# Kernel tuning notes

Measured on AMD Instinct MI355X. Metric: run time of the kernel, lower is better.

## Reference

```python
import jax, jax.numpy as jnp
import numpy as np

def setup_inputs() -> dict:
    key = jax.random.key(0)
    k1, k2 = jax.random.split(key)
    user_embeddings = jax.random.normal(k1, (1024, 64), dtype=jnp.float32)
    movie_embeddings = jax.random.normal(k2, (50000, 64), dtype=jnp.float32)
    return {"user_embeddings": user_embeddings, "movie_embeddings": movie_embeddings}

def reference(user_embeddings, movie_embeddings):
    # square_of_sum[b,m] = (sum_k u[b,k] m[m,k])^2
    square_of_sum = jnp.matmul(user_embeddings, movie_embeddings.T) ** 2
    # sum_of_square[b,m] = sum_k (u[b,k] m[m,k])^2 = (u^2) @ (m^2)^T
    # Algebraically identical to the original's broadcast (B, M, D) intermediate,
    # but computed as a second GEMM on squared embeddings.
    sum_of_square = jnp.matmul(user_embeddings ** 2, (movie_embeddings ** 2).T)
    interaction = 0.5 * (square_of_sum - sum_of_square)
    return interaction
```

## Files before the change

kernel.cpp:

```cpp
#include <hip/hip_runtime.h>

typedef short short8 __attribute__((ext_vector_type(8)));
typedef float f32x4 __attribute__((ext_vector_type(4)));

#define DK 64
#define BM 64
#define BN 128

__device__ __forceinline__ short f2bf(float x) {
    unsigned u = __builtin_bit_cast(unsigned, x);
    unsigned r = (u + 0x7fffu + ((u >> 16) & 1u)) >> 16;
    return (short)r;
}

__device__ __forceinline__ short8 sq8(short8 v) {
    short8 r;
#pragma unroll
    for (int i = 0; i < 8; ++i) {
        unsigned u = ((unsigned)(unsigned short)v[i]) << 16;
        float f = __builtin_bit_cast(float, u);
        unsigned p = __builtin_bit_cast(unsigned, f * f);
        r[i] = (short)((p + 0x8000u) >> 16);
    }
    return r;
}

__device__ __forceinline__ void gl_lds16(const void* g, void* l) {
    __builtin_amdgcn_global_load_lds(
        (const __attribute__((address_space(1))) unsigned int*)g,
        (__attribute__((address_space(3))) unsigned int*)l, 16, 0, 0);
}

__global__ __launch_bounds__(256)
void fm_convert(const float* __restrict__ U, const float* __restrict__ M,
                short* __restrict__ ws, int NU, int NM, int NUP, int NMP) {
    int id = blockIdx.x * blockDim.x + threadIdx.x;
    int total = (NUP + NMP) * 8;
    if (id >= total) return;
    int rowg = id >> 3;
    int p = id & 7;
    const float* src; short* dv; int row, nvalid;
    if (rowg < NUP) {
        row = rowg; src = U; dv = ws; nvalid = NU;
    } else {
        row = rowg - NUP; src = M;
        dv = ws + (size_t)NUP * DK; nvalid = NM;
    }
    short8 v8 = {0,0,0,0,0,0,0,0};
    if (row < nvalid) {
        const int cp = p ^ (row & 7);
        const float* s = src + (size_t)row * DK + cp * 8;
        float4 a = *(const float4*)(s);
        float4 b = *(const float4*)(s + 4);
        v8 = (short8){ f2bf(a.x), f2bf(a.y), f2bf(a.z), f2bf(a.w),
                       f2bf(b.x), f2bf(b.y), f2bf(b.z), f2bf(b.w) };
    }
    *(short8*)(dv + (size_t)row * DK + p * 8) = v8;
}

__global__ __launch_bounds__(256, 6)
void fm_gemm(const short* __restrict__ ws, float* __restrict__ out,
             int NM, int NMP, int NUP) {
    __shared__ short sA[BM * DK];
    __shared__ short sB[BN * DK];

    const int t = threadIdx.x;
    const int lane = t & 63;
    const int w = t >> 6;
    const int lr = lane & 15;
    const int lk = lane >> 4;

    const int ub  = blockIdx.x * BM;
    const int nb0 = blockIdx.y * BN;

    const short* gU = ws;
    const short* gM = ws + (size_t)NUP * DK;

    {
        const short* srcA = gU + (size_t)ub * DK;
        const short* srcB = gM + (size_t)nb0 * DK;
        const int lo = lane * 8;
#pragma unroll
        for (int j = 0; j < 2; ++j) {
            const int ch = w * 2 + j;
            gl_lds16(srcA + ch * 512 + lo, &sA[ch * 512]);
        }
#pragma unroll
        for (int j = 0; j < 4; ++j) {
            const int ch = w * 4 + j;
            gl_lds16(srcB + ch * 512 + lo, &sB[ch * 512]);
        }
    }
    __syncthreads();

    short8 bv[2][2];
#pragma unroll
    for (int n = 0; n < 2; ++n)
#pragma unroll
        for (int ks = 0; ks < 2; ++ks) {
            const int row = w * 32 + n * 16 + lr;
            const int c = ks * 4 + lk;
            const int idx = row * DK + ((c ^ (row & 7)) << 3);
            bv[n][ks] = *(const short8*)&sB[idx];
        }

    const int nbW = nb0 + w * 32;

#pragma unroll
    for (int m = 0; m < 4; ++m) {
        short8 av0, av1, aq0, aq1;
        {
            const int row = m * 16 + lr;
            const int i0 = row * DK + (((0 * 4 + lk) ^ (row & 7)) << 3);
            const int i1 = row * DK + (((1 * 4 + lk) ^ (row & 7)) << 3);
            av0 = *(const short8*)&sA[i0];
            av1 = *(const short8*)&sA[i1];
            aq0 = sq8(av0);
            aq1 = sq8(av1);
        }

        f32x4 s[2], q[2];
#pragma unroll
        for (int n = 0; n < 2; ++n) {
            s[n] = (f32x4){0.f, 0.f, 0.f, 0.f};
            q[n] = (f32x4){0.f, 0.f, 0.f, 0.f};
        }
#pragma unroll
        for (int n = 0; n < 2; ++n) {
            const short8 bq0 = sq8(bv[n][0]);
            const short8 bq1 = sq8(bv[n][1]);
            s[n] = __builtin_amdgcn_mfma_f32_16x16x32_bf16(bv[n][0], av0, s[n], 0, 0, 0);
            s[n] = __builtin_amdgcn_mfma_f32_16x16x32_bf16(bv[n][1], av1, s[n], 0, 0, 0);
            q[n] = __builtin_amdgcn_mfma_f32_16x16x32_bf16(bq0, aq0, q[n], 0, 0, 0);
            q[n] = __builtin_amdgcn_mfma_f32_16x16x32_bf16(bq1, aq1, q[n], 0, 0, 0);
        }

        float* rowp = out + (size_t)(ub + m * 16 + lr) * NM;
#pragma unroll
        for (int n = 0; n < 2; ++n) {
            const int col = nbW + n * 16 + lk * 4;
            if (col < NM) {
                f32x4 sv = s[n], qv = q[n];
                f32x4 rr;
#pragma unroll
                for (int j = 0; j < 4; ++j)
                    rr[j] = 0.5f * (sv[j] * sv[j] - qv[j]);
                *(f32x4*)(rowp + col) = rr;
            }
        }
    }
}

__global__ __launch_bounds__(256, 2)
void fm_fallback(const float* __restrict__ U, const float* __restrict__ M,
                 float* __restrict__ out, int NU, int NM) {
    __shared__ short sA [128 * DK];
    __shared__ short sA2[128 * DK];
    __shared__ short sB [128 * DK];
    __shared__ short sB2[128 * DK];

    const int t = threadIdx.x;
    const int lane = t & 63;
    const int w = t >> 6;
    const int wr = w >> 1;
    const int wc = w & 1;
    const int lr = lane & 15;
    const int lk = lane >> 4;

    const int mbase = blockIdx.x * 128;
    const int nbase = blockIdx.y * 128;

    const int r0 = t >> 4;
    const int c4 = t & 15;
    const int chunk = c4 >> 1;
    const int sub = c4 & 1;

    typedef short short4v __attribute__((ext_vector_type(4)));
#pragma unroll
    for (int i = 0; i < 8; ++i) {
        const int r = r0 + i * 16;
        const int sidx = r * DK + ((chunk ^ (r & 7)) << 3) + (sub << 2);
        {
            float4 v = make_float4(0.f, 0.f, 0.f, 0.f);
            const int gr = mbase + r;
            if (gr < NU) v = *(const float4*)(U + (size_t)gr * DK + c4 * 4);
            short4v b  = { f2bf(v.x), f2bf(v.y), f2bf(v.z), f2bf(v.w) };
            short4v b2 = { f2bf(v.x*v.x), f2bf(v.y*v.y), f2bf(v.z*v.z), f2bf(v.w*v.w) };
            *(short4v*)&sA[sidx] = b; *(short4v*)&sA2[sidx] = b2;
        }
        {
            float4 v = make_float4(0.f, 0.f, 0.f, 0.f);
            const int gr = nbase + r;
            if (gr < NM) v = *(const float4*)(M + (size_t)gr * DK + c4 * 4);
            short4v b  = { f2bf(v.x), f2bf(v.y), f2bf(v.z), f2bf(v.w) };
            short4v b2 = { f2bf(v.x*v.x), f2bf(v.y*v.y), f2bf(v.z*v.z), f2bf(v.w*v.w) };
            *(short4v*)&sB[sidx] = b; *(short4v*)&sB2[sidx] = b2;
        }
    }
    __syncthreads();

    f32x4 accS[4][4], accQ[4][4];
#pragma unroll
    for (int m = 0; m < 4; ++m)
#pragma unroll
        for (int n = 0; n < 4; ++n) {
            accS[m][n] = (f32x4){0.f,0.f,0.f,0.f};
            accQ[m][n] = (f32x4){0.f,0.f,0.f,0.f};
        }
#pragma unroll
    for (int ks = 0; ks < 2; ++ks) {
        short8 af[4], a2f[4], bfr[4], b2f[4];
        const int c = ks * 4 + lk;
#pragma unroll
        for (int m = 0; m < 4; ++m) {
            const int row = wr * 64 + m * 16 + lr;
            const int idx = row * DK + ((c ^ (row & 7)) << 3);
            af[m] = *(const short8*)&sA[idx]; a2f[m] = *(const short8*)&sA2[idx];
        }
#pragma unroll
        for (int n = 0; n < 4; ++n) {
            const int row = wc * 64 + n * 16 + lr;
            const int idx = row * DK + ((c ^ (row & 7)) << 3);
            bfr[n] = *(const short8*)&sB[idx]; b2f[n] = *(const short8*)&sB2[idx];
        }
#pragma unroll
        for (int m = 0; m < 4; ++m)
#pragma unroll
            for (int n = 0; n < 4; ++n) {
                accS[m][n] = __builtin_amdgcn_mfma_f32_16x16x32_bf16(af[m],  bfr[n], accS[m][n], 0, 0, 0);
                accQ[m][n] = __builtin_amdgcn_mfma_f32_16x16x32_bf16(a2f[m], b2f[n], accQ[m][n], 0, 0, 0);
            }
    }
#pragma unroll
    for (int m = 0; m < 4; ++m) {
        const int grow0 = mbase + wr * 64 + m * 16 + lk * 4;
#pragma unroll
        for (int n = 0; n < 4; ++n) {
            const int gcol = nbase + wc * 64 + n * 16 + lr;
            if (gcol < NM) {
                f32x4 s = accS[m][n]; f32x4 q = accQ[m][n];
#pragma unroll
                for (int r = 0; r < 4; ++r) {
                    const int grow = grow0 + r;
                    if (grow < NU)
                        out[(size_t)grow * NM + gcol] = 0.5f * (s[r]*s[r] - q[r]);
                }
            }
        }
    }
}

extern "C" void kernel_launch(void* const* d_in, const int* in_sizes, int n_in,
                              void* d_out, int out_size, void* d_ws, size_t ws_size,
                              hipStream_t stream) {
    const float* U = (const float*)d_in[0];
    const float* M = (const float*)d_in[1];
    float* out = (float*)d_out;
    const int NU = in_sizes[0] / DK;
    const int NM = in_sizes[1] / DK;
    const int NUP = NU;
    const int NMP = ((NM + BN - 1) / BN) * BN;
    const size_t need = (size_t)(NUP + NMP) * DK * sizeof(short);

    if ((NU % BM == 0) && (NM % 4 == 0) && ws_size >= need) {
        short* ws = (short*)d_ws;
        const int tasks = (NUP + NMP) * 8;
        fm_convert<<<(tasks + 255) / 256, 256, 0, stream>>>(U, M, ws, NU, NM, NUP, NMP);
        dim3 grid(NU / BM, NMP / BN);
        fm_gemm<<<grid, dim3(256), 0, stream>>>(ws, out, NM, NMP, NUP);
    } else {
        dim3 grid((NU + 127) / 128, (NM + 127) / 128);
        fm_fallback<<<grid, dim3(256), 0, stream>>>(U, M, out, NU, NM);
    }
}
```

Baseline: 50.62 us.

## Load GEMM operands directly from global memory instead of staging through LDS

```diff
diff --git a/kernel.cpp b/kernel.cpp
--- a/kernel.cpp
+++ b/kernel.cpp
@@ -23,12 +23,6 @@
         r[i] = (short)((p + 0x8000u) >> 16);
     }
     return r;
-}
-
-__device__ __forceinline__ void gl_lds16(const void* g, void* l) {
-    __builtin_amdgcn_global_load_lds(
-        (const __attribute__((address_space(1))) unsigned int*)g,
-        (__attribute__((address_space(3))) unsigned int*)l, 16, 0, 0);
 }
 
 __global__ __launch_bounds__(256)
@@ -48,8 +42,7 @@
     }
     short8 v8 = {0,0,0,0,0,0,0,0};
     if (row < nvalid) {
-        const int cp = p ^ (row & 7);
-        const float* s = src + (size_t)row * DK + cp * 8;
+        const float* s = src + (size_t)row * DK + p * 8;
         float4 a = *(const float4*)(s);
         float4 b = *(const float4*)(s + 4);
         v8 = (short8){ f2bf(a.x), f2bf(a.y), f2bf(a.z), f2bf(a.w),
@@ -58,12 +51,9 @@
     *(short8*)(dv + (size_t)row * DK + p * 8) = v8;
 }
 
-__global__ __launch_bounds__(256, 6)
+__global__ __launch_bounds__(256, 4)
 void fm_gemm(const short* __restrict__ ws, float* __restrict__ out,
              int NM, int NMP, int NUP) {
-    __shared__ short sA[BM * DK];
-    __shared__ short sB[BN * DK];
-
     const int t = threadIdx.x;
     const int lane = t & 63;
     const int w = t >> 6;
@@ -76,48 +66,24 @@
     const short* gU = ws;
     const short* gM = ws + (size_t)NUP * DK;
 
-    {
-        const short* srcA = gU + (size_t)ub * DK;
-        const short* srcB = gM + (size_t)nb0 * DK;
-        const int lo = lane * 8;
-#pragma unroll
-        for (int j = 0; j < 2; ++j) {
-            const int ch = w * 2 + j;
-            gl_lds16(srcA + ch * 512 + lo, &sA[ch * 512]);
-        }
-#pragma unroll
-        for (int j = 0; j < 4; ++j) {
-            const int ch = w * 4 + j;
-            gl_lds16(srcB + ch * 512 + lo, &sB[ch * 512]);
-        }
-    }
-    __syncthreads();
-
     short8 bv[2][2];
 #pragma unroll
     for (int n = 0; n < 2; ++n)
 #pragma unroll
         for (int ks = 0; ks < 2; ++ks) {
-            const int row = w * 32 + n * 16 + lr;
-            const int c = ks * 4 + lk;
-            const int idx = row * DK + ((c ^ (row & 7)) << 3);
-            bv[n][ks] = *(const short8*)&sB[idx];
+            const int row = nb0 + w * 32 + n * 16 + lr;
+            bv[n][ks] = *(const short8*)(gM + (size_t)row * DK + (ks * 4 + lk) * 8);
         }
 
     const int nbW = nb0 + w * 32;
 
 #pragma unroll
     for (int m = 0; m < 4; ++m) {
-        short8 av0, av1, aq0, aq1;
-        {
-            const int row = m * 16 + lr;
-            const int i0 = row * DK + (((0 * 4 + lk) ^ (row & 7)) << 3);
-            const int i1 = row * DK + (((1 * 4 + lk) ^ (row & 7)) << 3);
-            av0 = *(const short8*)&sA[i0];
-            av1 = *(const short8*)&sA[i1];
-            aq0 = sq8(av0);
-            aq1 = sq8(av1);
-        }
+        const int arow = ub + m * 16 + lr;
+        const short8 av0 = *(const short8*)(gU + (size_t)arow * DK + lk * 8);
+        const short8 av1 = *(const short8*)(gU + (size_t)arow * DK + (4 + lk) * 8);
+        const short8 aq0 = sq8(av0);
+        const short8 aq1 = sq8(av1);
 
         f32x4 s[2], q[2];
 #pragma unroll
@@ -135,7 +101,7 @@
             q[n] = __builtin_amdgcn_mfma_f32_16x16x32_bf16(bq1, aq1, q[n], 0, 0, 0);
         }
 
-        float* rowp = out + (size_t)(ub + m * 16 + lr) * NM;
+        float* rowp = out + (size_t)arow * NM;
 #pragma unroll
         for (int n = 0; n < 2; ++n) {
             const int col = nbW + n * 16 + lk * 4;
```

New measurement: 56.78 us. 1.12x slower.

## Fuse bf16 conversion into GEMM kernel, dropping separate convert pass

Applied to the files above, without the earlier changes.

```diff
diff --git a/kernel.cpp b/kernel.cpp
--- a/kernel.cpp
+++ b/kernel.cpp
@@ -25,42 +25,16 @@
     return r;
 }
 
-__device__ __forceinline__ void gl_lds16(const void* g, void* l) {
-    __builtin_amdgcn_global_load_lds(
-        (const __attribute__((address_space(1))) unsigned int*)g,
-        (__attribute__((address_space(3))) unsigned int*)l, 16, 0, 0);
-}
-
-__global__ __launch_bounds__(256)
-void fm_convert(const float* __restrict__ U, const float* __restrict__ M,
-                short* __restrict__ ws, int NU, int NM, int NUP, int NMP) {
-    int id = blockIdx.x * blockDim.x + threadIdx.x;
-    int total = (NUP + NMP) * 8;
-    if (id >= total) return;
-    int rowg = id >> 3;
-    int p = id & 7;
-    const float* src; short* dv; int row, nvalid;
-    if (rowg < NUP) {
-        row = rowg; src = U; dv = ws; nvalid = NU;
-    } else {
-        row = rowg - NUP; src = M;
-        dv = ws + (size_t)NUP * DK; nvalid = NM;
-    }
-    short8 v8 = {0,0,0,0,0,0,0,0};
-    if (row < nvalid) {
-        const int cp = p ^ (row & 7);
-        const float* s = src + (size_t)row * DK + cp * 8;
-        float4 a = *(const float4*)(s);
-        float4 b = *(const float4*)(s + 4);
-        v8 = (short8){ f2bf(a.x), f2bf(a.y), f2bf(a.z), f2bf(a.w),
-                       f2bf(b.x), f2bf(b.y), f2bf(b.z), f2bf(b.w) };
-    }
-    *(short8*)(dv + (size_t)row * DK + p * 8) = v8;
-}
-
-__global__ __launch_bounds__(256, 6)
-void fm_gemm(const short* __restrict__ ws, float* __restrict__ out,
-             int NM, int NMP, int NUP) {
+__device__ __forceinline__ short8 cvt8(const float* s) {
+    float4 a = *(const float4*)(s);
+    float4 b = *(const float4*)(s + 4);
+    return (short8){ f2bf(a.x), f2bf(a.y), f2bf(a.z), f2bf(a.w),
+                     f2bf(b.x), f2bf(b.y), f2bf(b.z), f2bf(b.w) };
+}
+
+__global__ __launch_bounds__(256, 4)
+void fm_fused(const float* __restrict__ U, const float* __restrict__ M,
+              float* __restrict__ out, int NU, int NM) {
     __shared__ short sA[BM * DK];
     __shared__ short sB[BN * DK];
 
@@ -73,23 +47,24 @@
     const int ub  = blockIdx.x * BM;
     const int nb0 = blockIdx.y * BN;
 
-    const short* gU = ws;
-    const short* gM = ws + (size_t)NUP * DK;
-
-    {
-        const short* srcA = gU + (size_t)ub * DK;
-        const short* srcB = gM + (size_t)nb0 * DK;
-        const int lo = lane * 8;
-#pragma unroll
-        for (int j = 0; j < 2; ++j) {
-            const int ch = w * 2 + j;
-            gl_lds16(srcA + ch * 512 + lo, &sA[ch * 512]);
-        }
-#pragma unroll
-        for (int j = 0; j < 4; ++j) {
-            const int ch = w * 4 + j;
-            gl_lds16(srcB + ch * 512 + lo, &sB[ch * 512]);
-        }
+#pragma unroll
+    for (int j = 0; j < 2; ++j) {
+        const int idx = t + 256 * j;
+        const int row = idx >> 3;
+        const int p = idx & 7;
+        short8 v = cvt8(U + (size_t)(ub + row) * DK + p * 8);
+        *(short8*)&sA[row * DK + ((p ^ (row & 7)) << 3)] = v;
+    }
+#pragma unroll
+    for (int j = 0; j < 4; ++j) {
+        const int idx = t + 256 * j;
+        const int row = idx >> 3;
+        const int p = idx & 7;
+        const int grow = nb0 + row;
+        short8 v = {0,0,0,0,0,0,0,0};
+        if (grow < NM)
+            v = cvt8(M + (size_t)grow * DK + p * 8);
+        *(short8*)&sB[row * DK + ((p ^ (row & 7)) << 3)] = v;
     }
     __syncthreads();
 
@@ -258,16 +233,11 @@
     float* out = (float*)d_out;
     const int NU = in_sizes[0] / DK;
     const int NM = in_sizes[1] / DK;
-    const int NUP = NU;
     const int NMP = ((NM + BN - 1) / BN) * BN;
-    const size_t need = (size_t)(NUP + NMP) * DK * sizeof(short);
-
-    if ((NU % BM == 0) && (NM % 4 == 0) && ws_size >= need) {
-        short* ws = (short*)d_ws;
-        const int tasks = (NUP + NMP) * 8;
-        fm_convert<<<(tasks + 255) / 256, 256, 0, stream>>>(U, M, ws, NU, NM, NUP, NMP);
+
+    if ((NU % BM == 0) && (NM % 4 == 0)) {
         dim3 grid(NU / BM, NMP / BN);
-        fm_gemm<<<grid, dim3(256), 0, stream>>>(ws, out, NM, NMP, NUP);
+        fm_fused<<<grid, dim3(256), 0, stream>>>(U, M, out, NU, NM);
     } else {
         dim3 grid((NU + 127) / 128, (NM + 127) / 128);
         fm_fallback<<<grid, dim3(256), 0, stream>>>(U, M, out, NU, NM);
```

New measurement: 52.31 us. +3.4%, slower.
